# Kernel optimization log

Hardware: AMD Instinct MI355X
Metric: run time of the kernel (lower is better)

## Reference

```python
import jax, jax.numpy as jnp
import numpy as np

B, S, NX, H = 8, 1024, 1024, 16
HD = NX // H  # head dim = 64
MASKED_BIAS = -10000.0


def setup_inputs() -> dict:
    key = jax.random.key(0)
    ks = jax.random.split(key, 6)
    return {
        "x": jax.random.normal(ks[0], (B, S, NX), dtype=jnp.float32),
        "query": jax.random.normal(ks[1], (B, S, NX), dtype=jnp.float32),
        "c_attn_w": jax.random.normal(ks[2], (NX, 3 * NX), dtype=jnp.float32) * 0.02,
        "c_attn_b": jnp.zeros((3 * NX,), dtype=jnp.float32),
        "c_proj_w": jax.random.normal(ks[3], (NX, NX), dtype=jnp.float32) * 0.02,
        "c_proj_b": jnp.zeros((NX,), dtype=jnp.float32),
    }


def _split_heads(t):
    # [B, S, NX] -> [B, H, S, HD]
    b, s, _ = t.shape
    return t.reshape(b, s, H, HD).transpose(0, 2, 1, 3)


def reference(x, query, c_attn_w, c_attn_b, c_proj_w, c_proj_b):
    # Conv1D: y = x @ W + b
    kv = x @ c_attn_w + c_attn_b          # [B,S,3NX]; use key/value slices
    qy = query @ c_attn_w + c_attn_b      # [B,S,3NX]; use query slice
    q = _split_heads(qy[..., :NX])                     # [B,H,S,HD]
    k = _split_heads(kv[..., NX:2 * NX])               # [B,H,S,HD]
    v = _split_heads(kv[..., 2 * NX:])                 # [B,H,S,HD]

    w = jnp.einsum("bhqd,bhkd->bhqk", q, k) / jnp.sqrt(jnp.float32(HD))
    causal = jnp.tril(jnp.ones((S, S), dtype=bool))[None, None]
    w = jnp.where(causal, w, jnp.float32(MASKED_BIAS))
    w = jax.nn.softmax(w, axis=-1)
    a = jnp.einsum("bhqk,bhkd->bhqd", w, v)            # [B,H,S,HD]
    a = a.transpose(0, 2, 1, 3).reshape(B, S, NX)      # merge heads
    return a @ c_proj_w + c_proj_b
```

## Files before the change

### kernel.cpp

```cpp
#include <hip/hip_runtime.h>
#include <cstdint>
#include <cstddef>

#define Bb   8
#define Ss   1024
#define NXx  1024
#define Hh   16
#define HDd  64
#define Mm   (Bb*Ss)

typedef __bf16 bf16x8 __attribute__((ext_vector_type(8)));
typedef float  f32x4  __attribute__((ext_vector_type(4)));

__device__ __forceinline__ unsigned short f2bf(float f) {
    union { float f; unsigned int u; } v; v.f = f;
    unsigned int r = v.u + 0x7fffu + ((v.u >> 16) & 1u);
    return (unsigned short)(r >> 16);
}

__device__ __forceinline__ void load_lds16(const unsigned short* g, unsigned short* lds_base) {
    __builtin_amdgcn_global_load_lds(
        (const __attribute__((address_space(1))) void*)g,
        (__attribute__((address_space(3))) void*)lds_base, 16, 0, 0);
}

__global__ void cast_f32_bf16(const float* __restrict__ in,
                              unsigned short* __restrict__ out, int n) {
    int i = (blockIdx.x * blockDim.x + threadIdx.x) * 4;
    if (i >= n) return;
    const float4 v = *(const float4*)(in + i);
    unsigned long long p = (unsigned long long)f2bf(v.x)
        | ((unsigned long long)f2bf(v.y) << 16)
        | ((unsigned long long)f2bf(v.z) << 32)
        | ((unsigned long long)f2bf(v.w) << 48);
    *(unsigned long long*)(out + i) = p;
}

__global__ void transpose_cast(const float* __restrict__ in,
                               unsigned short* __restrict__ out, int R, int C) {
    __shared__ float tile[32][33];
    int c0 = blockIdx.x * 32, r0 = blockIdx.y * 32;
    for (int i = threadIdx.y; i < 32; i += 8)
        tile[i][threadIdx.x] = in[(size_t)(r0 + i) * C + c0 + threadIdx.x];
    __syncthreads();
    for (int i = threadIdx.y; i < 32; i += 8)
        out[(size_t)(c0 + i) * R + r0 + threadIdx.x] = f2bf(tile[threadIdx.x][i]);
}

__global__ __launch_bounds__(256) void gemm128(
    const unsigned short* __restrict__ Ax,
    const unsigned short* __restrict__ Aq,
    const unsigned short* __restrict__ Bt,
    const float* __restrict__ bias,
    int K, int mode,
    unsigned short* __restrict__ out_q,
    unsigned short* __restrict__ out_k,
    unsigned short* __restrict__ out_v,
    float* __restrict__ out_f)
{
    __shared__ unsigned short smem[8192];
    unsigned short (*As)[32] = (unsigned short (*)[32])(smem);
    unsigned short (*Bs)[32] = (unsigned short (*)[32])(smem + 4096);

    const int tid  = threadIdx.x;
    const int w    = tid >> 6;
    const int lane = tid & 63;

    const int nx   = (mode == 0) ? 24 : 8;
    const int nxh  = nx >> 1;
    const int n    = blockIdx.x;
    const int xcd  = n & 7;
    const int sgrp = n >> 3;
    const int m0   = ((xcd >> 1) * 16 + sgrp / nxh) * 128;
    const int n0   = ((xcd & 1) * nxh + sgrp % nxh) * 128;
    const int region = n0 >> 10;
    const unsigned short* A = (mode == 0 && region == 0) ? Aq : Ax;

    const int wm   = (w >> 1) * 64;
    const int wn   = (w & 1) * 64;
    const int lrow = lane & 15;
    const int quad = lane >> 4;

    f32x4 acc[4][4] = {};

    const int srow = w * 16 + (lane >> 2);
    const int scol = (((lane & 3) ^ ((lane >> 3) & 3)) << 3);
    const unsigned short* Ag0 = A  + (size_t)(m0 + srow) * K + scol;
    const unsigned short* Ag1 = Ag0 + (size_t)64 * K;
    const unsigned short* Bg0 = Bt + (size_t)(n0 + srow) * K + scol;
    const unsigned short* Bg1 = Bg0 + (size_t)64 * K;
    unsigned short* ldsA0 = &As[w * 16][0];
    unsigned short* ldsA1 = &As[64 + w * 16][0];
    unsigned short* ldsB0 = &Bs[w * 16][0];
    unsigned short* ldsB1 = &Bs[64 + w * 16][0];

    const int fc = ((quad ^ ((lrow >> 1) & 3)) << 3);

    for (int k0 = 0; k0 < K; k0 += 32) {
        __syncthreads();
        load_lds16(Ag0 + k0, ldsA0);
        load_lds16(Ag1 + k0, ldsA1);
        load_lds16(Bg0 + k0, ldsB0);
        load_lds16(Bg1 + k0, ldsB1);
        __syncthreads();

        bf16x8 af[4], bfr[4];
#pragma unroll
        for (int i = 0; i < 4; ++i) {
            af[i]  = *(const bf16x8*)&As[wm + i * 16 + lrow][fc];
            bfr[i] = *(const bf16x8*)&Bs[wn + i * 16 + lrow][fc];
        }
#pragma unroll
        for (int i = 0; i < 4; ++i)
#pragma unroll
            for (int j = 0; j < 4; ++j)
                acc[i][j] = __builtin_amdgcn_mfma_f32_16x16x32_bf16(af[i], bfr[j], acc[i][j], 0, 0, 0);
    }

    __syncthreads();

    if (mode == 1) {
#pragma unroll
        for (int i = 0; i < 4; ++i)
#pragma unroll
            for (int j = 0; j < 4; ++j) {
                const int ncol = n0 + wn + j * 16 + lrow;
                const float bv = bias[ncol];
#pragma unroll
                for (int r = 0; r < 4; ++r) {
                    const int mrow = m0 + wm + i * 16 + quad * 4 + r;
                    out_f[(size_t)mrow * NXx + ncol] = acc[i][j][r] + bv;
                }
            }
        return;
    }

    unsigned short* ep = smem + w * 1536;

    if (region != 2) {
        unsigned short* outp = (region == 0) ? out_q : out_k;
#pragma unroll
        for (int j = 0; j < 4; ++j) {
            const float bv = bias[n0 + wn + j * 16 + lrow];
#pragma unroll
            for (int i = 0; i < 4; ++i)
#pragma unroll
                for (int r = 0; r < 4; ++r)
                    ep[(i * 16 + quad * 4 + r) * 24 + lrow] = f2bf(acc[i][j][r] + bv);
#pragma unroll
            for (int t = 0; t < 2; ++t) {
                const int c    = t * 64 + lane;
                const int row  = c >> 1, ch = (c & 1) * 8;
                const int mrow = m0 + wm + row;
                const int cc   = (n0 + wn + j * 16 + ch) & (NXx - 1);
                const int hh   = cc >> 6, dd = cc & 63;
                const int bh   = (mrow >> 10) * Hh + hh;
                const int ss   = mrow & (Ss - 1);
                *(uint4*)&outp[((size_t)bh * Ss + ss) * HDd + dd] =
                    *(const uint4*)&ep[row * 24 + ch];
            }
        }
    } else {
#pragma unroll
        for (int j = 0; j < 4; ++j) {
            const float bv = bias[n0 + wn + j * 16 + lrow];
#pragma unroll
            for (int i = 0; i < 4; ++i)
#pragma unroll
                for (int r = 0; r < 4; ++r)
                    ep[lrow * 72 + i * 16 + quad * 4 + r] = f2bf(acc[i][j][r] + bv);
#pragma unroll
            for (int t = 0; t < 2; ++t) {
                const int c    = t * 64 + lane;
                const int col  = c >> 3, rc = (c & 7) * 8;
                const int cc   = (n0 + wn + j * 16 + col) & (NXx - 1);
                const int hh   = cc >> 6, dd = cc & 63;
                const int mrow = m0 + wm + rc;
                const int bh   = (mrow >> 10) * Hh + hh;
                const int ss   = mrow & (Ss - 1);
                *(uint4*)&out_v[((size_t)bh * HDd + dd) * Ss + ss] =
                    *(const uint4*)&ep[col * 72 + rc];
            }
        }
    }
}

__global__ __launch_bounds__(256) void flash_attn(
    const unsigned short* __restrict__ Qh,
    const unsigned short* __restrict__ Kh,
    const unsigned short* __restrict__ Vt,
    unsigned short* __restrict__ about)
{
    __shared__ unsigned short Ks[64][64];
    __shared__ unsigned short Vs[64][64];
    __shared__ unsigned short Pl[4][16][72];

    const int tid  = threadIdx.x;
    const int w    = tid >> 6;
    const int lane = tid & 63;
    const int bh   = blockIdx.x & 127;
    const int pr   = blockIdx.x >> 7;
    const int b    = bh >> 4, h = bh & 15;
    const int lrow = lane & 15;
    const int quad = lane >> 4;

    const unsigned short* Qb = Qh + (size_t)bh * Ss * HDd;
    const unsigned short* Kb = Kh + (size_t)bh * Ss * HDd;
    const unsigned short* Vb = Vt + (size_t)bh * HDd * Ss;

    const int sr = w * 16 + (lane >> 3);
    const int lc = (((lane & 7) ^ ((lane >> 3) & 7)) << 3);
    unsigned short* ldsK0 = &Ks[w * 16][0];
    unsigned short* ldsK1 = &Ks[w * 16 + 8][0];
    unsigned short* ldsV0 = &Vs[w * 16][0];
    unsigned short* ldsV1 = &Vs[w * 16 + 8][0];

    const int ca = ((quad ^ (lrow & 7)) << 3);
    const int cb = (((4 | quad) ^ (lrow & 7)) << 3);

    for (int half = 0; half < 2; ++half) {
        const int qt    = half ? (15 - pr) : pr;
        const int qBase = qt * 64 + w * 16;

        const bf16x8 aq0 = *(const bf16x8*)(Qb + (size_t)(qBase + lrow) * HDd + quad * 8);
        const bf16x8 aq1 = *(const bf16x8*)(Qb + (size_t)(qBase + lrow) * HDd + 32 + quad * 8);

        f32x4 O[4] = {};
        float lsum[4] = { 0.f, 0.f, 0.f, 0.f };

        const int nkt = qt + 1;
        for (int kt = 0; kt < nkt; ++kt) {
            const int k0 = kt * 64;

            __syncthreads();
            load_lds16(Kb + (size_t)(k0 + sr) * HDd + lc,     ldsK0);
            load_lds16(Kb + (size_t)(k0 + sr + 8) * HDd + lc, ldsK1);
            load_lds16(Vb + (size_t)sr * Ss + k0 + lc,        ldsV0);
            load_lds16(Vb + (size_t)(sr + 8) * Ss + k0 + lc,  ldsV1);
            __syncthreads();

            f32x4 s[4] = {};
#pragma unroll
            for (int j = 0; j < 4; ++j) {
                bf16x8 b0 = *(const bf16x8*)&Ks[j * 16 + lrow][ca];
                bf16x8 b1 = *(const bf16x8*)&Ks[j * 16 + lrow][cb];
                s[j] = __builtin_amdgcn_mfma_f32_16x16x32_bf16(aq0, b0, s[j], 0, 0, 0);
                s[j] = __builtin_amdgcn_mfma_f32_16x16x32_bf16(aq1, b1, s[j], 0, 0, 0);
            }

            const bool diag = (kt == qt);
#pragma unroll
            for (int r = 0; r < 4; ++r) {
                const int q = qBase + quad * 4 + r;
#pragma unroll
                for (int j = 0; j < 4; ++j) {
                    float e = __expf(s[j][r] * 0.125f);
                    if (diag && (k0 + j * 16 + lrow > q)) e = 0.f;
                    lsum[r] += e;
                    Pl[w][quad * 4 + r][j * 16 + lrow] = f2bf(e);
                }
            }
            __syncthreads();

            const bf16x8 ap0 = *(const bf16x8*)&Pl[w][lrow][quad * 8];
            const bf16x8 ap1 = *(const bf16x8*)&Pl[w][lrow][32 + quad * 8];
#pragma unroll
            for (int f = 0; f < 4; ++f) {
                bf16x8 bv0 = *(const bf16x8*)&Vs[f * 16 + lrow][ca];
                bf16x8 bv1 = *(const bf16x8*)&Vs[f * 16 + lrow][cb];
                O[f] = __builtin_amdgcn_mfma_f32_16x16x32_bf16(ap0, bv0, O[f], 0, 0, 0);
                O[f] = __builtin_amdgcn_mfma_f32_16x16x32_bf16(ap1, bv1, O[f], 0, 0, 0);
            }
        }

#pragma unroll
        for (int r = 0; r < 4; ++r) {
            float l = lsum[r];
            l += __shfl_xor(l, 1);
            l += __shfl_xor(l, 2);
            l += __shfl_xor(l, 4);
            l += __shfl_xor(l, 8);
            const float inv = 1.0f / l;
            const int q = qBase + quad * 4 + r;
            const size_t base = ((size_t)b * Ss + q) * NXx + h * HDd;
#pragma unroll
            for (int f = 0; f < 4; ++f)
                about[base + f * 16 + lrow] = f2bf(O[f][r] * inv);
        }
    }
}

extern "C" void kernel_launch(void* const* d_in, const int* in_sizes, int n_in,
                              void* d_out, int out_size, void* d_ws, size_t ws_size,
                              hipStream_t stream) {
    const float* x        = (const float*)d_in[0];
    const float* query    = (const float*)d_in[1];
    const float* c_attn_w = (const float*)d_in[2];
    const float* c_attn_b = (const float*)d_in[3];
    const float* c_proj_w = (const float*)d_in[4];
    const float* c_proj_b = (const float*)d_in[5];
    float* out = (float*)d_out;

    const size_t nTok = (size_t)Mm * NXx;
    char* ws = (char*)d_ws;
    unsigned short* xb    = (unsigned short*)ws;                 ws += nTok * 2;
    unsigned short* qb    = (unsigned short*)ws;                 ws += nTok * 2;
    unsigned short* Wt    = (unsigned short*)ws;                 ws += (size_t)3 * NXx * NXx * 2;
    unsigned short* Pt    = (unsigned short*)ws;                 ws += (size_t)NXx * NXx * 2;
    unsigned short* Qh    = (unsigned short*)ws;                 ws += nTok * 2;
    unsigned short* Kh    = (unsigned short*)ws;                 ws += nTok * 2;
    unsigned short* Vt    = (unsigned short*)ws;                 ws += nTok * 2;
    unsigned short* about = (unsigned short*)ws;                 ws += nTok * 2;
    if ((size_t)(ws - (char*)d_ws) > ws_size) return;

    const int nElem = (int)nTok;
    cast_f32_bf16<<<nElem / 4 / 256, 256, 0, stream>>>(x, xb, nElem);
    cast_f32_bf16<<<nElem / 4 / 256, 256, 0, stream>>>(query, qb, nElem);
    transpose_cast<<<dim3(96, 32), dim3(32, 8), 0, stream>>>(c_attn_w, Wt, NXx, 3 * NXx);
    transpose_cast<<<dim3(32, 32), dim3(32, 8), 0, stream>>>(c_proj_w, Pt, NXx, NXx);

    gemm128<<<dim3(24 * 64), 256, 0, stream>>>(xb, qb, Wt, c_attn_b, NXx, 0,
                                               Qh, Kh, Vt, nullptr);
    flash_attn<<<1024, 256, 0, stream>>>(Qh, Kh, Vt, about);

    gemm128<<<dim3(8 * 64), 256, 0, stream>>>(about, nullptr, Pt, c_proj_b, NXx, 1,
                                              nullptr, nullptr, nullptr, out);
}
```

Before: 291.1 us.

## Fuse prep kernels, double GEMM K-tile, rework LDS swizzles, drop attention barrier

Merges the two casts and two weight transposes into a single prep launch to remove launch overhead. The GEMM now stages a 64-wide K slice per iteration, halving the number of barrier pairs at the cost of doubling LDS use. The LDS swizzles in the GEMM and attention are changed, and a __syncthreads before the per-warp P reads is removed, relying on each warp reading only its own Pl slice. The bf16 rounding is simplified from round-to-nearest-even to round-half-up, which changes numerics slightly.

New measurement: 264.9 us. 1.1x faster.

```diff
diff --git a/kernel.cpp b/kernel.cpp
--- a/kernel.cpp
+++ b/kernel.cpp
@@ -14,8 +14,7 @@
 
 __device__ __forceinline__ unsigned short f2bf(float f) {
     union { float f; unsigned int u; } v; v.f = f;
-    unsigned int r = v.u + 0x7fffu + ((v.u >> 16) & 1u);
-    return (unsigned short)(r >> 16);
+    return (unsigned short)((v.u + 0x8000u) >> 16);
 }
 
 __device__ __forceinline__ void load_lds16(const unsigned short* g, unsigned short* lds_base) {
@@ -24,27 +23,42 @@
         (__attribute__((address_space(3))) void*)lds_base, 16, 0, 0);
 }
 
-__global__ void cast_f32_bf16(const float* __restrict__ in,
-                              unsigned short* __restrict__ out, int n) {
-    int i = (blockIdx.x * blockDim.x + threadIdx.x) * 4;
-    if (i >= n) return;
-    const float4 v = *(const float4*)(in + i);
-    unsigned long long p = (unsigned long long)f2bf(v.x)
-        | ((unsigned long long)f2bf(v.y) << 16)
-        | ((unsigned long long)f2bf(v.z) << 32)
-        | ((unsigned long long)f2bf(v.w) << 48);
-    *(unsigned long long*)(out + i) = p;
-}
-
-__global__ void transpose_cast(const float* __restrict__ in,
-                               unsigned short* __restrict__ out, int R, int C) {
+__global__ __launch_bounds__(256) void prep(
+    const float* __restrict__ x, const float* __restrict__ query,
+    const float* __restrict__ caw, const float* __restrict__ cpw,
+    unsigned short* __restrict__ xb, unsigned short* __restrict__ qb,
+    unsigned short* __restrict__ Wt, unsigned short* __restrict__ Pt)
+{
     __shared__ float tile[32][33];
-    int c0 = blockIdx.x * 32, r0 = blockIdx.y * 32;
-    for (int i = threadIdx.y; i < 32; i += 8)
-        tile[i][threadIdx.x] = in[(size_t)(r0 + i) * C + c0 + threadIdx.x];
+    const int bid = blockIdx.x;
+    const int tid = threadIdx.x;
+
+    if (bid < 16384) {
+        const float* in = (bid < 8192) ? x : query;
+        unsigned short* out = (bid < 8192) ? xb : qb;
+        const int i = ((bid & 8191) * 256 + tid) * 4;
+        const float4 v = *(const float4*)(in + i);
+        unsigned long long p = (unsigned long long)f2bf(v.x)
+            | ((unsigned long long)f2bf(v.y) << 16)
+            | ((unsigned long long)f2bf(v.z) << 32)
+            | ((unsigned long long)f2bf(v.w) << 48);
+        *(unsigned long long*)(out + i) = p;
+        return;
+    }
+
+    const float* in;
+    unsigned short* out;
+    int C, t;
+    if (bid < 16384 + 3072) { in = caw; out = Wt; C = 3072; t = bid - 16384; }
+    else                    { in = cpw; out = Pt; C = 1024; t = bid - 19456; }
+    const int ntx = C >> 5;
+    const int c0 = (t % ntx) * 32, r0 = (t / ntx) * 32;
+    const int tx = tid & 31, ty = tid >> 5;
+    for (int i = ty; i < 32; i += 8)
+        tile[i][tx] = in[(size_t)(r0 + i) * C + c0 + tx];
     __syncthreads();
-    for (int i = threadIdx.y; i < 32; i += 8)
-        out[(size_t)(c0 + i) * R + r0 + threadIdx.x] = f2bf(tile[threadIdx.x][i]);
+    for (int i = ty; i < 32; i += 8)
+        out[(size_t)(c0 + i) * 1024 + r0 + tx] = f2bf(tile[tx][i]);
 }
 
 __global__ __launch_bounds__(256) void gemm128(
@@ -58,9 +72,9 @@
     unsigned short* __restrict__ out_v,
     float* __restrict__ out_f)
 {
-    __shared__ unsigned short smem[8192];
-    unsigned short (*As)[32] = (unsigned short (*)[32])(smem);
-    unsigned short (*Bs)[32] = (unsigned short (*)[32])(smem + 4096);
+    __shared__ unsigned short smem[16384];
+    unsigned short (*As)[64] = (unsigned short (*)[64])(smem);
+    unsigned short (*Bs)[64] = (unsigned short (*)[64])(smem + 8192);
 
     const int tid  = threadIdx.x;
     const int w    = tid >> 6;
@@ -83,38 +97,38 @@
 
     f32x4 acc[4][4] = {};
 
-    const int srow = w * 16 + (lane >> 2);
-    const int scol = (((lane & 3) ^ ((lane >> 3) & 3)) << 3);
-    const unsigned short* Ag0 = A  + (size_t)(m0 + srow) * K + scol;
-    const unsigned short* Ag1 = Ag0 + (size_t)64 * K;
-    const unsigned short* Bg0 = Bt + (size_t)(n0 + srow) * K + scol;
-    const unsigned short* Bg1 = Bg0 + (size_t)64 * K;
-    unsigned short* ldsA0 = &As[w * 16][0];
-    unsigned short* ldsA1 = &As[64 + w * 16][0];
-    unsigned short* ldsB0 = &Bs[w * 16][0];
-    unsigned short* ldsB1 = &Bs[64 + w * 16][0];
-
-    const int fc = ((quad ^ ((lrow >> 1) & 3)) << 3);
-
-    for (int k0 = 0; k0 < K; k0 += 32) {
+    const int rr   = lane >> 3;
+    const int scol = (((lane & 7) ^ ((lane >> 4) & 3)) << 3);
+    const unsigned short* Ag = A  + (size_t)(m0 + w * 32 + rr) * K + scol;
+    const unsigned short* Bg = Bt + (size_t)(n0 + w * 32 + rr) * K + scol;
+    unsigned short* ldsA = smem + (w * 32) * 64;
+    unsigned short* ldsB = smem + 8192 + (w * 32) * 64;
+
+    const int sw = (lrow >> 1) & 3;
+
+    for (int k0 = 0; k0 < K; k0 += 64) {
         __syncthreads();
-        load_lds16(Ag0 + k0, ldsA0);
-        load_lds16(Ag1 + k0, ldsA1);
-        load_lds16(Bg0 + k0, ldsB0);
-        load_lds16(Bg1 + k0, ldsB1);
+#pragma unroll
+        for (int c = 0; c < 4; ++c) {
+            load_lds16(Ag + (size_t)(c * 8) * K + k0, ldsA + c * 512);
+            load_lds16(Bg + (size_t)(c * 8) * K + k0, ldsB + c * 512);
+        }
         __syncthreads();
-
-        bf16x8 af[4], bfr[4];
-#pragma unroll
-        for (int i = 0; i < 4; ++i) {
-            af[i]  = *(const bf16x8*)&As[wm + i * 16 + lrow][fc];
-            bfr[i] = *(const bf16x8*)&Bs[wn + i * 16 + lrow][fc];
-        }
-#pragma unroll
-        for (int i = 0; i < 4; ++i)
-#pragma unroll
-            for (int j = 0; j < 4; ++j)
-                acc[i][j] = __builtin_amdgcn_mfma_f32_16x16x32_bf16(af[i], bfr[j], acc[i][j], 0, 0, 0);
+#pragma unroll
+        for (int kk = 0; kk < 2; ++kk) {
+            bf16x8 af[4], bfr[4];
+            const int pc = (((kk * 4 + quad) ^ sw) << 3);
+#pragma unroll
+            for (int i = 0; i < 4; ++i) {
+                af[i]  = *(const bf16x8*)&As[wm + i * 16 + lrow][pc];
+                bfr[i] = *(const bf16x8*)&Bs[wn + i * 16 + lrow][pc];
+            }
+#pragma unroll
+            for (int i = 0; i < 4; ++i)
+#pragma unroll
+                for (int j = 0; j < 4; ++j)
+                    acc[i][j] = __builtin_amdgcn_mfma_f32_16x16x32_bf16(af[i], bfr[j], acc[i][j], 0, 0, 0);
+        }
     }
 
     __syncthreads();
@@ -135,7 +149,7 @@
         return;
     }
 
-    unsigned short* ep = smem + w * 1536;
+    unsigned short* ep = smem + w * 2048;
 
     if (region != 2) {
         unsigned short* outp = (region == 0) ? out_q : out_k;
@@ -208,15 +222,16 @@
     const unsigned short* Kb = Kh + (size_t)bh * Ss * HDd;
     const unsigned short* Vb = Vt + (size_t)bh * HDd * Ss;
 
-    const int sr = w * 16 + (lane >> 3);
-    const int lc = (((lane & 7) ^ ((lane >> 3) & 7)) << 3);
+    const int sr = lane >> 3;
+    const int lc = (((lane & 7) ^ ((lane >> 4) & 3)) << 3);
     unsigned short* ldsK0 = &Ks[w * 16][0];
     unsigned short* ldsK1 = &Ks[w * 16 + 8][0];
     unsigned short* ldsV0 = &Vs[w * 16][0];
     unsigned short* ldsV1 = &Vs[w * 16 + 8][0];
 
-    const int ca = ((quad ^ (lrow & 7)) << 3);
-    const int cb = (((4 | quad) ^ (lrow & 7)) << 3);
+    const int sw = (lrow >> 1) & 3;
+    const int ca = ((quad ^ sw) << 3);
+    const int cb = (((4 + quad) ^ sw) << 3);
 
     for (int half = 0; half < 2; ++half) {
         const int qt    = half ? (15 - pr) : pr;
@@ -233,10 +248,10 @@
             const int k0 = kt * 64;
 
             __syncthreads();
-            load_lds16(Kb + (size_t)(k0 + sr) * HDd + lc,     ldsK0);
-            load_lds16(Kb + (size_t)(k0 + sr + 8) * HDd + lc, ldsK1);
-            load_lds16(Vb + (size_t)sr * Ss + k0 + lc,        ldsV0);
-            load_lds16(Vb + (size_t)(sr + 8) * Ss + k0 + lc,  ldsV1);
+            load_lds16(Kb + (size_t)(k0 + w * 16 + sr) * HDd + lc,     ldsK0);
+            load_lds16(Kb + (size_t)(k0 + w * 16 + sr + 8) * HDd + lc, ldsK1);
+            load_lds16(Vb + (size_t)(w * 16 + sr) * Ss + k0 + lc,      ldsV0);
+            load_lds16(Vb + (size_t)(w * 16 + sr + 8) * Ss + k0 + lc,  ldsV1);
             __syncthreads();
 
             f32x4 s[4] = {};
@@ -260,7 +275,6 @@
                     Pl[w][quad * 4 + r][j * 16 + lrow] = f2bf(e);
                 }
             }
-            __syncthreads();
 
             const bf16x8 ap0 = *(const bf16x8*)&Pl[w][lrow][quad * 8];
             const bf16x8 ap1 = *(const bf16x8*)&Pl[w][lrow][32 + quad * 8];
@@ -313,11 +327,7 @@
     unsigned short* about = (unsigned short*)ws;                 ws += nTok * 2;
     if ((size_t)(ws - (char*)d_ws) > ws_size) return;
 
-    const int nElem = (int)nTok;
-    cast_f32_bf16<<<nElem / 4 / 256, 256, 0, stream>>>(x, xb, nElem);
-    cast_f32_bf16<<<nElem / 4 / 256, 256, 0, stream>>>(query, qb, nElem);
-    transpose_cast<<<dim3(96, 32), dim3(32, 8), 0, stream>>>(c_attn_w, Wt, NXx, 3 * NXx);
-    transpose_cast<<<dim3(32, 32), dim3(32, 8), 0, stream>>>(c_proj_w, Pt, NXx, NXx);
+    prep<<<20480, 256, 0, stream>>>(x, query, c_attn_w, c_proj_w, xb, qb, Wt, Pt);
 
     gemm128<<<dim3(24 * 64), 256, 0, stream>>>(xb, qb, Wt, c_attn_b, NXx, 0,
                                                Qh, Kh, Vt, nullptr);
```
